# Kernel optimization log

Hardware: AMD Instinct MI355X
Metric: run time of the kernel (lower is better)

## Reference

```python
import jax, jax.numpy as jnp
import numpy as np
import math

B, S, E = 4, 2048, 1024
H, D = 16, 64

def setup_inputs() -> dict:
    key = jax.random.key(0)
    ks = jax.random.split(key, 9)
    sE = 1.0 / math.sqrt(E)
    sHD = 1.0 / math.sqrt(H * D)
    return {
        "x": jax.random.normal(ks[0], (B, S, E), jnp.float32),
        "Wq": jax.random.normal(ks[1], (H, E, D), jnp.float32) * sE,
        "bq": jax.random.normal(ks[2], (H, D), jnp.float32) * sE,
        "Wk": jax.random.normal(ks[3], (H, E, D), jnp.float32) * sE,
        "bk": jax.random.normal(ks[4], (H, D), jnp.float32) * sE,
        "Wv": jax.random.normal(ks[5], (H, E, D), jnp.float32) * sE,
        "bv": jax.random.normal(ks[6], (H, D), jnp.float32) * sE,
        "Wo": jax.random.normal(ks[7], (E, E), jnp.float32) * sHD,
        "bo": jax.random.normal(ks[8], (E,), jnp.float32) * sHD,
    }

def reference(x, Wq, bq, Wk, bk, Wv, bv, Wo, bo):
    # Projections for all heads at once: [B,H,S,D]
    Q = jnp.einsum('bse,hed->bhsd', x, Wq) + bq[:, None, :]
    K = jnp.einsum('bse,hed->bhsd', x, Wk) + bk[:, None, :]
    V = jnp.einsum('bse,hed->bhsd', x, Wv) + bv[:, None, :]
    scale = 1.0 / math.sqrt(D)
    scores = jnp.einsum('bhsd,bhtd->bhst', Q, K) * scale  # [B,H,S,S]
    S_len = x.shape[1]
    causal = jnp.tril(jnp.ones((S_len, S_len), dtype=bool))
    scores = jnp.where(causal, scores, -jnp.inf)
    probs = jax.nn.softmax(scores, axis=-1)
    ctx = jnp.einsum('bhst,bhtd->bhsd', probs, V)  # [B,H,S,D]
    # concat heads: head order matches torch cat over ModuleList
    conc = jnp.transpose(ctx, (0, 2, 1, 3)).reshape(x.shape[0], S_len, H * D)
    # torch Linear: y = conc @ W.T + b ; Wo stored as [out,in]=[E,E]
    out = conc @ Wo.T + bo
    # dropout is identity in eval mode
    return out
```

## Files before the change

kernel.cpp:

```cpp
#include <hip/hip_runtime.h>
#include <math.h>

constexpr int Bn = 4;
constexpr int Sn = 2048;
constexpr int En = 1024;
constexpr int Hn = 16;
constexpr int Dn = 64;

typedef float f32x4 __attribute__((ext_vector_type(4)));
typedef short s16x8 __attribute__((ext_vector_type(8)));
typedef short s16x4 __attribute__((ext_vector_type(4)));

__device__ __forceinline__ short f2bf(float f) {
    unsigned u = __builtin_bit_cast(unsigned, f);
    unsigned r = (u + 0x7fffu + ((u >> 16) & 1u)) >> 16;
    return (short)r;
}

__device__ __forceinline__ unsigned cvt_pk_bf16(float lo, float hi) {
    unsigned r;
    asm("v_cvt_pk_bf16_f32 %0, %1, %2" : "=v"(r) : "v"(lo), "v"(hi));
    return r;
}

__device__ __forceinline__ void glds16(const short* g, short* l) {
    __builtin_amdgcn_global_load_lds(
        (const __attribute__((address_space(1))) short*)g,
        (__attribute__((address_space(3))) short*)l, 16, 0, 0);
}

__global__ __launch_bounds__(256) void prep_kernel(
    const float* __restrict__ x, short* __restrict__ y,
    const float* __restrict__ Wq, const float* __restrict__ bq,
    const float* __restrict__ Wk, const float* __restrict__ bk,
    const float* __restrict__ Wv, const float* __restrict__ bv,
    short* __restrict__ Wcat, float* __restrict__ bias_cat,
    const float* __restrict__ Wo, short* __restrict__ Wob)
{
    const int bid = blockIdx.x;
    const int tid = threadIdx.x;

    if (bid < 8192) {
        size_t i = ((size_t)bid * 256 + tid) * 4;
        float4 v = *(const float4*)(x + i);
        s16x4 o;
        o[0] = f2bf(v.x); o[1] = f2bf(v.y); o[2] = f2bf(v.z); o[3] = f2bf(v.w);
        *(s16x4*)(y + i) = o;
    } else if (bid < 8960) {
        const int j  = bid - 8192;
        const int et = j & 15, h = (j >> 4) & 15, p = j >> 8;
        const float* W  = (p == 0) ? Wq : (p == 1) ? Wk : Wv;
        const float* bb = (p == 0) ? bq : (p == 1) ? bk : bv;
        const float* Wh = W + (size_t)h * En * Dn;

        __shared__ float T[64][65];
        #pragma unroll
        for (int it = 0; it < 16; it++) {
            int idx = tid + it * 256;
            int e = idx >> 6, d = idx & 63;
            T[d][e] = Wh[(size_t)(et * 64 + e) * Dn + d];
        }
        __syncthreads();
        #pragma unroll
        for (int it = 0; it < 16; it++) {
            int idx = tid + it * 256;
            int d = idx >> 6, e = idx & 63;
            Wcat[(size_t)(p * 1024 + h * 64 + d) * En + et * 64 + e] = f2bf(T[d][e]);
        }
        if (et == 0 && tid < 64)
            bias_cat[p * 1024 + h * 64 + tid] = bb[h * 64 + tid];
    } else {
        const size_t base = (size_t)(bid - 8960) * En;
        #pragma unroll
        for (int i = 0; i < 4; i++) {
            int k = tid + i * 256;
            Wob[base + k] = f2bf(Wo[base + k]);
        }
    }
}

__global__ __launch_bounds__(512) void gemm_bt_kernel(
    const short* __restrict__ A,
    const short* __restrict__ Bt,
    const float* __restrict__ bias,
    float* __restrict__ outF,
    short* __restrict__ Qb, short* __restrict__ Kb, short* __restrict__ Vtb,
    int mode)
{
    constexpr int K = En;
    const int m0 = blockIdx.x * 256;
    const int n0 = blockIdx.y * 128;

    __shared__ short As[256 * 64];
    __shared__ short Bs[128 * 64];

    const int tid  = threadIdx.x;
    const int w    = tid >> 6;
    const int lane = tid & 63;
    const int quad = lane >> 4;
    const int l15  = lane & 15;
    const int wr = (w >> 1) * 64;
    const int wc = (w & 1) * 64;

    f32x4 acc[4][4];
    #pragma unroll
    for (int i = 0; i < 4; i++)
        #pragma unroll
        for (int j = 0; j < 4; j++)
            #pragma unroll
            for (int e = 0; e < 4; e++) acc[i][j][e] = 0.f;

    for (int k0 = 0; k0 < K; k0 += 64) {
        #pragma unroll
        for (int r = 0; r < 4; r++) {
            int c   = (r * 8 + w) * 64 + lane;
            int row = c >> 3;
            int lp  = (c & 7) ^ (row & 7);
            glds16(A + (size_t)(m0 + row) * K + k0 + lp * 8,
                   As + (r * 8 + w) * 512);
        }
        #pragma unroll
        for (int r = 0; r < 2; r++) {
            int c   = (r * 8 + w) * 64 + lane;
            int row = c >> 3;
            int lp  = (c & 7) ^ (row & 7);
            glds16(Bt + (size_t)(n0 + row) * K + k0 + lp * 8,
                   Bs + (r * 8 + w) * 512);
        }
        __syncthreads();

        #pragma unroll
        for (int ks = 0; ks < 2; ks++) {
            s16x8 af[4], bfr[4];
            #pragma unroll
            for (int mt = 0; mt < 4; mt++) {
                int row = wr + mt * 16 + l15;
                af[mt] = *(const s16x8*)&As[row * 64 + (((ks * 4 + quad) ^ (l15 & 7)) * 8)];
            }
            #pragma unroll
            for (int nt = 0; nt < 4; nt++) {
                int row = wc + nt * 16 + l15;
                bfr[nt] = *(const s16x8*)&Bs[row * 64 + (((ks * 4 + quad) ^ (l15 & 7)) * 8)];
            }
            #pragma unroll
            for (int mt = 0; mt < 4; mt++)
                #pragma unroll
                for (int nt = 0; nt < 4; nt++)
                    acc[mt][nt] = __builtin_amdgcn_mfma_f32_16x16x32_bf16(
                        af[mt], bfr[nt], acc[mt][nt], 0, 0, 0);
        }
        __syncthreads();
    }

    if (mode == 0) {
        #pragma unroll
        for (int mt = 0; mt < 4; mt++) {
            #pragma unroll
            for (int reg = 0; reg < 4; reg++) {
                int m = m0 + wr + mt * 16 + quad * 4 + reg;
                #pragma unroll
                for (int nt = 0; nt < 4; nt++) {
                    int n = n0 + wc + nt * 16 + l15;
                    outF[(size_t)m * En + n] = acc[mt][nt][reg] + bias[n];
                }
            }
        }
    } else {
        const int p = (n0 + wc) >> 10;
        if (p < 2) {
            const float qs = (p == 0) ? 0.125f * 1.44269504088896f : 1.0f;
            short* dst = (p == 0) ? Qb : Kb;
            #pragma unroll
            for (int mt = 0; mt < 4; mt++) {
                #pragma unroll
                for (int reg = 0; reg < 4; reg++) {
                    int m = m0 + wr + mt * 16 + quad * 4 + reg;
                    int b = m >> 11, s = m & 2047;
                    #pragma unroll
                    for (int nt = 0; nt < 4; nt++) {
                        int n = n0 + wc + nt * 16 + l15;
                        int h = (n >> 6) & 15, d = n & 63;
                        dst[(((size_t)(b * Hn + h)) * Sn + s) * Dn + d] =
                            f2bf((acc[mt][nt][reg] + bias[n]) * qs);
                    }
                }
            }
        } else {
            #pragma unroll
            for (int mt = 0; mt < 4; mt++) {
                int m = m0 + wr + mt * 16 + quad * 4;
                int b = m >> 11, s = m & 2047;
                #pragma unroll
                for (int nt = 0; nt < 4; nt++) {
                    int n = n0 + wc + nt * 16 + l15;
                    int h = (n >> 6) & 15, d = n & 63;
                    s16x4 pk;
                    #pragma unroll
                    for (int reg = 0; reg < 4; reg++)
                        pk[reg] = f2bf(acc[mt][nt][reg] + bias[n]);
                    *(s16x4*)(Vtb + (((size_t)(b * Hn + h)) * Dn + d) * Sn + s) = pk;
                }
            }
        }
    }
}

__global__ __launch_bounds__(512) void gemm_bt_out_kernel(
    const short* __restrict__ A,
    const short* __restrict__ Bt,
    const float* __restrict__ bias,
    float* __restrict__ outF)
{
    constexpr int K = En;
    const int m0 = blockIdx.x * 128;
    const int n0 = blockIdx.y * 128;

    __shared__ short As[128 * 64];
    __shared__ short Bs[128 * 64];

    const int tid  = threadIdx.x;
    const int w    = tid >> 6;
    const int lane = tid & 63;
    const int quad = lane >> 4;
    const int l15  = lane & 15;
    const int wr = (w >> 1) * 32;
    const int wc = (w & 1) * 64;

    f32x4 acc[2][4];
    #pragma unroll
    for (int i = 0; i < 2; i++)
        #pragma unroll
        for (int j = 0; j < 4; j++)
            #pragma unroll
            for (int e = 0; e < 4; e++) acc[i][j][e] = 0.f;

    for (int k0 = 0; k0 < K; k0 += 64) {
        #pragma unroll
        for (int r = 0; r < 2; r++) {
            int c   = (r * 8 + w) * 64 + lane;
            int row = c >> 3;
            int lp  = (c & 7) ^ (row & 7);
            glds16(A + (size_t)(m0 + row) * K + k0 + lp * 8,
                   As + (r * 8 + w) * 512);
        }
        #pragma unroll
        for (int r = 0; r < 2; r++) {
            int c   = (r * 8 + w) * 64 + lane;
            int row = c >> 3;
            int lp  = (c & 7) ^ (row & 7);
            glds16(Bt + (size_t)(n0 + row) * K + k0 + lp * 8,
                   Bs + (r * 8 + w) * 512);
        }
        __syncthreads();

        #pragma unroll
        for (int ks = 0; ks < 2; ks++) {
            s16x8 af[2], bfr[4];
            #pragma unroll
            for (int mt = 0; mt < 2; mt++) {
                int row = wr + mt * 16 + l15;
                af[mt] = *(const s16x8*)&As[row * 64 + (((ks * 4 + quad) ^ (l15 & 7)) * 8)];
            }
            #pragma unroll
            for (int nt = 0; nt < 4; nt++) {
                int row = wc + nt * 16 + l15;
                bfr[nt] = *(const s16x8*)&Bs[row * 64 + (((ks * 4 + quad) ^ (l15 & 7)) * 8)];
            }
            #pragma unroll
            for (int mt = 0; mt < 2; mt++)
                #pragma unroll
                for (int nt = 0; nt < 4; nt++)
                    acc[mt][nt] = __builtin_amdgcn_mfma_f32_16x16x32_bf16(
                        af[mt], bfr[nt], acc[mt][nt], 0, 0, 0);
        }
        __syncthreads();
    }

    #pragma unroll
    for (int mt = 0; mt < 2; mt++) {
        #pragma unroll
        for (int reg = 0; reg < 4; reg++) {
            int m = m0 + wr + mt * 16 + quad * 4 + reg;
            #pragma unroll
            for (int nt = 0; nt < 4; nt++) {
                int n = n0 + wc + nt * 16 + l15;
                outF[(size_t)m * En + n] = acc[mt][nt][reg] + bias[n];
            }
        }
    }
}

__global__ __launch_bounds__(256, 8) void attn_mfma_kernel(
    const short* __restrict__ Q, const short* __restrict__ K,
    const short* __restrict__ Vt, short* __restrict__ Cb)
{
    constexpr int PP = 72;
    const int bid = blockIdx.x;
    const int kk  = bid >> 3;
    const int bh  = (bid & 7) * 8 + (kk >> 4);
    const int i   = kk & 15;
    const int b = bh >> 4, h = bh & 15;
    const int t0 = i, t1 = 31 - i;

    __shared__ short Ks[64 * 64];
    __shared__ short Vts[64 * 64];
    __shared__ short Ps[128 * PP];
    __shared__ float l_sh[128];

    const int tid  = threadIdx.x;
    const int w    = tid >> 6;
    const int lane = tid & 63;
    const int quad = lane >> 4;
    const int l15  = lane & 15;

    const short* Kp = K + (size_t)bh * Sn * Dn;
    const short* Vp = Vt + (size_t)bh * Dn * Sn;

    const int tf[2] = {t0, t1};
    s16x8 aq[2][2];
    #pragma unroll
    for (int f = 0; f < 2; f++)
        #pragma unroll
        for (int ks = 0; ks < 2; ks++)
            aq[f][ks] = *(const s16x8*)(
                Q + ((size_t)bh * Sn + tf[f] * 64 + w * 16 + l15) * Dn +
                ks * 32 + quad * 8);

    f32x4 acc[2][4];
    #pragma unroll
    for (int f = 0; f < 2; f++)
        #pragma unroll
        for (int nt = 0; nt < 4; nt++)
            #pragma unroll
            for (int e = 0; e < 4; e++) acc[f][nt][e] = 0.f;
    float lpart[2] = {0.f, 0.f};

    for (int kt = 0; kt <= t1; kt++) {
        #pragma unroll
        for (int r = 0; r < 2; r++) {
            int c   = (r * 4 + w) * 64 + lane;
            int row = c >> 3;
            int lp  = (c & 7) ^ (row & 7);
            glds16(Kp + (size_t)(kt * 64 + row) * Dn + lp * 8,
                   Ks + (r * 4 + w) * 512);
            glds16(Vp + (size_t)row * Sn + kt * 64 + lp * 8,
                   Vts + (r * 4 + w) * 512);
        }
        __syncthreads();

        #pragma unroll
        for (int f = 0; f < 2; f++) {
            if (kt > tf[f]) continue;
            f32x4 st[4];
            #pragma unroll
            for (int nt = 0; nt < 4; nt++)
                #pragma unroll
                for (int e = 0; e < 4; e++) st[nt][e] = 0.f;
            #pragma unroll
            for (int ks = 0; ks < 2; ks++) {
                #pragma unroll
                for (int nt = 0; nt < 4; nt++) {
                    s16x8 bk = *(const s16x8*)&Ks[(nt * 16 + l15) * 64 +
                                                  (((ks * 4 + quad) ^ (l15 & 7)) * 8)];
                    st[nt] = __builtin_amdgcn_mfma_f32_16x16x32_bf16(
                        bk, aq[f][ks], st[nt], 0, 0, 0);
                }
            }
            const bool diag = (kt == tf[f]);
            #pragma unroll
            for (int nt = 0; nt < 4; nt++) {
                float v[4];
                #pragma unroll
                for (int reg = 0; reg < 4; reg++) {
                    float e = __builtin_amdgcn_exp2f(st[nt][reg]);
                    if (diag && (nt * 16 + quad * 4 + reg) > (w * 16 + l15))
                        e = 0.f;
                    v[reg] = e;
                    lpart[f] += e;
                }
                uint2 pk;
                pk.x = cvt_pk_bf16(v[0], v[1]);
                pk.y = cvt_pk_bf16(v[2], v[3]);
                *(uint2*)&Ps[(f * 64 + w * 16 + l15) * PP + nt * 16 + quad * 4] = pk;
            }
        }

        #pragma unroll
        for (int ks = 0; ks < 2; ks++) {
            s16x8 bv[4];
            #pragma unroll
            for (int nt = 0; nt < 4; nt++)
                bv[nt] = *(const s16x8*)&Vts[(nt * 16 + l15) * 64 +
                                             (((ks * 4 + quad) ^ (l15 & 7)) * 8)];
            #pragma unroll
            for (int f = 0; f < 2; f++) {
                if (kt > tf[f]) continue;
                s16x8 ap = *(const s16x8*)&Ps[(f * 64 + w * 16 + l15) * PP +
                                              ks * 32 + quad * 8];
                #pragma unroll
                for (int nt = 0; nt < 4; nt++)
                    acc[f][nt] = __builtin_amdgcn_mfma_f32_16x16x32_bf16(
                        ap, bv[nt], acc[f][nt], 0, 0, 0);
            }
        }
        __syncthreads();
    }

    #pragma unroll
    for (int f = 0; f < 2; f++) {
        float l = lpart[f];
        l += __shfl_xor(l, 16);
        l += __shfl_xor(l, 32);
        if (quad == 0) l_sh[f * 64 + w * 16 + l15] = l;
    }
    __syncthreads();

    #pragma unroll
    for (int f = 0; f < 2; f++) {
        #pragma unroll
        for (int reg = 0; reg < 4; reg++) {
            int s = tf[f] * 64 + w * 16 + quad * 4 + reg;
            float inv = 1.f / l_sh[f * 64 + w * 16 + quad * 4 + reg];
            #pragma unroll
            for (int nt = 0; nt < 4; nt++) {
                int d = nt * 16 + l15;
                Cb[((size_t)(b * Sn + s)) * En + h * Dn + d] =
                    f2bf(acc[f][nt][reg] * inv);
            }
        }
    }
}

extern "C" void kernel_launch(void* const* d_in, const int* in_sizes, int n_in,
                              void* d_out, int out_size, void* d_ws, size_t ws_size,
                              hipStream_t stream) {
    const float* x  = (const float*)d_in[0];
    const float* Wq = (const float*)d_in[1];
    const float* bq = (const float*)d_in[2];
    const float* Wk = (const float*)d_in[3];
    const float* bk = (const float*)d_in[4];
    const float* Wv = (const float*)d_in[5];
    const float* bv = (const float*)d_in[6];
    const float* Wo = (const float*)d_in[7];
    const float* bo = (const float*)d_in[8];
    float* out = (float*)d_out;

    const size_t XS   = (size_t)Bn * Sn * En;
    const size_t WCS  = (size_t)3 * En * Hn * Dn;
    const size_t WOS  = (size_t)En * En;
    const size_t QSZ  = (size_t)Bn * Hn * Sn * Dn;

    short* Ax    = (short*)d_ws;
    short* Wcat  = Ax + XS;
    short* Wob   = Wcat + WCS;
    float* biasc = (float*)(Wob + WOS);
    short* Qb    = (short*)(biasc + 3072);
    short* Kb    = Qb + QSZ;
    short* Vtb   = Kb + QSZ;
    short* Cbf   = Vtb + QSZ;

    prep_kernel<<<dim3(8192 + 768 + 1024), 256, 0, stream>>>(
        x, Ax, Wq, bq, Wk, bk, Wv, bv, Wcat, biasc, Wo, Wob);

    gemm_bt_kernel<<<dim3((Bn * Sn) / 256, 3072 / 128), 512, 0, stream>>>(
        Ax, Wcat, biasc, nullptr, Qb, Kb, Vtb, 1);

    attn_mfma_kernel<<<dim3(16 * Bn * Hn), 256, 0, stream>>>(Qb, Kb, Vtb, Cbf);

    gemm_bt_out_kernel<<<dim3((Bn * Sn) / 128, En / 128), 512, 0, stream>>>(
        Cbf, Wob, bo, out);
}
```

Before: 244.9 us.

## Double-buffer K/V tiles in attention kernel with prefetch and vmcnt waits

The attention kernel now keeps two LDS buffers for K and V^T. It issues the global-to-LDS loads for tile kt+1 before computing on tile kt, waiting with s_waitcnt vmcnt(4) so that only the current tile's loads must finish. The aim is to hide global memory latency behind the MFMA and softmax work. The cost is double the K/V shared memory, which may lower occupancy under launch_bounds(256,8), and raw s_barrier with manual waitcnt is fragile if LDS write visibility is not guaranteed. The row sum is also reduced pairwise rather than serially.

After: 265.9 us. +8.6%, slower.

```diff
diff --git a/kernel.cpp b/kernel.cpp
--- a/kernel.cpp
+++ b/kernel.cpp
@@ -302,8 +302,8 @@
     const int b = bh >> 4, h = bh & 15;
     const int t0 = i, t1 = 31 - i;
 
-    __shared__ short Ks[64 * 64];
-    __shared__ short Vts[64 * 64];
+    __shared__ short Ks[2 * 64 * 64];
+    __shared__ short Vts[2 * 64 * 64];
     __shared__ short Ps[128 * PP];
     __shared__ float l_sh[128];
 
@@ -335,18 +335,37 @@
             for (int e = 0; e < 4; e++) acc[f][nt][e] = 0.f;
     float lpart[2] = {0.f, 0.f};
 
+    const int c0   = w * 64 + lane;
+    const int c1   = (4 + w) * 64 + lane;
+    const int row0 = c0 >> 3, lp0 = (c0 & 7) ^ (row0 & 7);
+    const int row1 = c1 >> 3, lp1 = (c1 & 7) ^ (row1 & 7);
+
+    #define STAGE(j, bufn)                                                    \
+        do {                                                                  \
+            glds16(Kp + (size_t)((j) * 64 + row0) * Dn + lp0 * 8,             \
+                   Ks + (bufn) * 4096 + w * 512);                             \
+            glds16(Vp + (size_t)row0 * Sn + (j) * 64 + lp0 * 8,               \
+                   Vts + (bufn) * 4096 + w * 512);                            \
+            glds16(Kp + (size_t)((j) * 64 + row1) * Dn + lp1 * 8,             \
+                   Ks + (bufn) * 4096 + (4 + w) * 512);                       \
+            glds16(Vp + (size_t)row1 * Sn + (j) * 64 + lp1 * 8,               \
+                   Vts + (bufn) * 4096 + (4 + w) * 512);                      \
+        } while (0)
+
+    STAGE(0, 0);
+
     for (int kt = 0; kt <= t1; kt++) {
-        #pragma unroll
-        for (int r = 0; r < 2; r++) {
-            int c   = (r * 4 + w) * 64 + lane;
-            int row = c >> 3;
-            int lp  = (c & 7) ^ (row & 7);
-            glds16(Kp + (size_t)(kt * 64 + row) * Dn + lp * 8,
-                   Ks + (r * 4 + w) * 512);
-            glds16(Vp + (size_t)row * Sn + kt * 64 + lp * 8,
-                   Vts + (r * 4 + w) * 512);
-        }
-        __syncthreads();
+        const int cur = kt & 1;
+        if (kt < t1) {
+            STAGE(kt + 1, cur ^ 1);
+            asm volatile("s_waitcnt vmcnt(4)" ::: "memory");
+        } else {
+            asm volatile("s_waitcnt vmcnt(0)" ::: "memory");
+        }
+        __builtin_amdgcn_s_barrier();
+
+        const short* Ksb  = Ks  + cur * 4096;
+        const short* Vtsb = Vts + cur * 4096;
 
         #pragma unroll
         for (int f = 0; f < 2; f++) {
@@ -360,8 +379,8 @@
             for (int ks = 0; ks < 2; ks++) {
                 #pragma unroll
                 for (int nt = 0; nt < 4; nt++) {
-                    s16x8 bk = *(const s16x8*)&Ks[(nt * 16 + l15) * 64 +
-                                                  (((ks * 4 + quad) ^ (l15 & 7)) * 8)];
+                    s16x8 bk = *(const s16x8*)&Ksb[(nt * 16 + l15) * 64 +
+                                                   (((ks * 4 + quad) ^ (l15 & 7)) * 8)];
                     st[nt] = __builtin_amdgcn_mfma_f32_16x16x32_bf16(
                         bk, aq[f][ks], st[nt], 0, 0, 0);
                 }
@@ -376,8 +395,8 @@
                     if (diag && (nt * 16 + quad * 4 + reg) > (w * 16 + l15))
                         e = 0.f;
                     v[reg] = e;
-                    lpart[f] += e;
                 }
+                lpart[f] += (v[0] + v[1]) + (v[2] + v[3]);
                 uint2 pk;
                 pk.x = cvt_pk_bf16(v[0], v[1]);
                 pk.y = cvt_pk_bf16(v[2], v[3]);
@@ -390,8 +409,8 @@
             s16x8 bv[4];
             #pragma unroll
             for (int nt = 0; nt < 4; nt++)
-                bv[nt] = *(const s16x8*)&Vts[(nt * 16 + l15) * 64 +
-                                             (((ks * 4 + quad) ^ (l15 & 7)) * 8)];
+                bv[nt] = *(const s16x8*)&Vtsb[(nt * 16 + l15) * 64 +
+                                              (((ks * 4 + quad) ^ (l15 & 7)) * 8)];
             #pragma unroll
             for (int f = 0; f < 2; f++) {
                 if (kt > tf[f]) continue;
@@ -403,8 +422,9 @@
                         ap, bv[nt], acc[f][nt], 0, 0, 0);
             }
         }
-        __syncthreads();
-    }
+        __builtin_amdgcn_s_barrier();
+    }
+    #undef STAGE
 
     #pragma unroll
     for (int f = 0; f < 2; f++) {
```

## Split paired causal query tiles into one tile per block, longest first

Applied to the files above, without the earlier changes.

The attention kernel previously gave each block a pair of query tiles (i and 31-i) so every block did balanced causal work while sharing each K/V tile load. Now each block handles a single 64-row query tile, and the grid doubles to 2048 blocks ordered so the longest tiles are dispatched first. This halves per-block LDS and register use, which can raise occupancy and improve scheduling. In exchange, K/V tiles are loaded once per query tile instead of once per pair, so global and L2 traffic increases.

Measured after the change: 241.9 us. Within noise of the previous version (-1.2%).

```diff
diff --git a/kernel.cpp b/kernel.cpp
--- a/kernel.cpp
+++ b/kernel.cpp
@@ -295,17 +295,17 @@
     const short* __restrict__ Vt, short* __restrict__ Cb)
 {
     constexpr int PP = 72;
-    const int bid = blockIdx.x;
-    const int kk  = bid >> 3;
-    const int bh  = (bid & 7) * 8 + (kk >> 4);
-    const int i   = kk & 15;
+    const int bid  = blockIdx.x;
+    const int slot = bid & 7;
+    const int j    = bid >> 3;
+    const int t    = 31 - (j >> 3);
+    const int bh   = slot * 8 + (j & 7);
     const int b = bh >> 4, h = bh & 15;
-    const int t0 = i, t1 = 31 - i;
 
     __shared__ short Ks[64 * 64];
     __shared__ short Vts[64 * 64];
-    __shared__ short Ps[128 * PP];
-    __shared__ float l_sh[128];
+    __shared__ short Ps[64 * PP];
+    __shared__ float l_sh[64];
 
     const int tid  = threadIdx.x;
     const int w    = tid >> 6;
@@ -316,26 +316,23 @@
     const short* Kp = K + (size_t)bh * Sn * Dn;
     const short* Vp = Vt + (size_t)bh * Dn * Sn;
 
-    const int tf[2] = {t0, t1};
-    s16x8 aq[2][2];
-    #pragma unroll
-    for (int f = 0; f < 2; f++)
-        #pragma unroll
-        for (int ks = 0; ks < 2; ks++)
-            aq[f][ks] = *(const s16x8*)(
-                Q + ((size_t)bh * Sn + tf[f] * 64 + w * 16 + l15) * Dn +
-                ks * 32 + quad * 8);
-
-    f32x4 acc[2][4];
-    #pragma unroll
-    for (int f = 0; f < 2; f++)
-        #pragma unroll
-        for (int nt = 0; nt < 4; nt++)
-            #pragma unroll
-            for (int e = 0; e < 4; e++) acc[f][nt][e] = 0.f;
-    float lpart[2] = {0.f, 0.f};
-
-    for (int kt = 0; kt <= t1; kt++) {
+    s16x8 aq[2];
+    #pragma unroll
+    for (int ks = 0; ks < 2; ks++)
+        aq[ks] = *(const s16x8*)(
+            Q + ((size_t)bh * Sn + t * 64 + w * 16 + l15) * Dn +
+            ks * 32 + quad * 8);
+
+    f32x4 acc[4];
+    #pragma unroll
+    for (int nt = 0; nt < 4; nt++)
+        #pragma unroll
+        for (int e = 0; e < 4; e++) acc[nt][e] = 0.f;
+    float lpart = 0.f;
+
+    const int prow = (w * 16 + l15) * PP;
+
+    for (int kt = 0; kt <= t; kt++) {
         #pragma unroll
         for (int r = 0; r < 2; r++) {
             int c   = (r * 4 + w) * 64 + lane;
@@ -348,85 +345,71 @@
         }
         __syncthreads();
 
-        #pragma unroll
-        for (int f = 0; f < 2; f++) {
-            if (kt > tf[f]) continue;
-            f32x4 st[4];
-            #pragma unroll
-            for (int nt = 0; nt < 4; nt++)
-                #pragma unroll
-                for (int e = 0; e < 4; e++) st[nt][e] = 0.f;
-            #pragma unroll
-            for (int ks = 0; ks < 2; ks++) {
-                #pragma unroll
-                for (int nt = 0; nt < 4; nt++) {
-                    s16x8 bk = *(const s16x8*)&Ks[(nt * 16 + l15) * 64 +
-                                                  (((ks * 4 + quad) ^ (l15 & 7)) * 8)];
-                    st[nt] = __builtin_amdgcn_mfma_f32_16x16x32_bf16(
-                        bk, aq[f][ks], st[nt], 0, 0, 0);
-                }
-            }
-            const bool diag = (kt == tf[f]);
+        f32x4 st[4];
+        #pragma unroll
+        for (int nt = 0; nt < 4; nt++)
+            #pragma unroll
+            for (int e = 0; e < 4; e++) st[nt][e] = 0.f;
+        #pragma unroll
+        for (int ks = 0; ks < 2; ks++) {
             #pragma unroll
             for (int nt = 0; nt < 4; nt++) {
-                float v[4];
-                #pragma unroll
-                for (int reg = 0; reg < 4; reg++) {
-                    float e = __builtin_amdgcn_exp2f(st[nt][reg]);
-                    if (diag && (nt * 16 + quad * 4 + reg) > (w * 16 + l15))
-                        e = 0.f;
-                    v[reg] = e;
-                    lpart[f] += e;
-                }
-                uint2 pk;
-                pk.x = cvt_pk_bf16(v[0], v[1]);
-                pk.y = cvt_pk_bf16(v[2], v[3]);
-                *(uint2*)&Ps[(f * 64 + w * 16 + l15) * PP + nt * 16 + quad * 4] = pk;
-            }
+                s16x8 bk = *(const s16x8*)&Ks[(nt * 16 + l15) * 64 +
+                                              (((ks * 4 + quad) ^ (l15 & 7)) * 8)];
+                st[nt] = __builtin_amdgcn_mfma_f32_16x16x32_bf16(
+                    bk, aq[ks], st[nt], 0, 0, 0);
+            }
+        }
+
+        const bool diag = (kt == t);
+        #pragma unroll
+        for (int nt = 0; nt < 4; nt++) {
+            float v[4];
+            #pragma unroll
+            for (int reg = 0; reg < 4; reg++) {
+                float e = __builtin_amdgcn_exp2f(st[nt][reg]);
+                if (diag && (nt * 16 + quad * 4 + reg) > (w * 16 + l15))
+                    e = 0.f;
+                v[reg] = e;
+                lpart += e;
+            }
+            uint2 pk;
+            pk.x = cvt_pk_bf16(v[0], v[1]);
+            pk.y = cvt_pk_bf16(v[2], v[3]);
+            *(uint2*)&Ps[prow + nt * 16 + quad * 4] = pk;
         }
 
         #pragma unroll
         for (int ks = 0; ks < 2; ks++) {
-            s16x8 bv[4];
-            #pragma unroll
-            for (int nt = 0; nt < 4; nt++)
-                bv[nt] = *(const s16x8*)&Vts[(nt * 16 + l15) * 64 +
-                                             (((ks * 4 + quad) ^ (l15 & 7)) * 8)];
-            #pragma unroll
-            for (int f = 0; f < 2; f++) {
-                if (kt > tf[f]) continue;
-                s16x8 ap = *(const s16x8*)&Ps[(f * 64 + w * 16 + l15) * PP +
-                                              ks * 32 + quad * 8];
-                #pragma unroll
-                for (int nt = 0; nt < 4; nt++)
-                    acc[f][nt] = __builtin_amdgcn_mfma_f32_16x16x32_bf16(
-                        ap, bv[nt], acc[f][nt], 0, 0, 0);
-            }
-        }
-        __syncthreads();
-    }
-
-    #pragma unroll
-    for (int f = 0; f < 2; f++) {
-        float l = lpart[f];
+            s16x8 ap = *(const s16x8*)&Ps[prow + ks * 32 + quad * 8];
+            #pragma unroll
+            for (int nt = 0; nt < 4; nt++) {
+                s16x8 bv = *(const s16x8*)&Vts[(nt * 16 + l15) * 64 +
+                                               (((ks * 4 + quad) ^ (l15 & 7)) * 8)];
+                acc[nt] = __builtin_amdgcn_mfma_f32_16x16x32_bf16(
+                    ap, bv, acc[nt], 0, 0, 0);
+            }
+        }
+        __syncthreads();
+    }
+
+    {
+        float l = lpart;
         l += __shfl_xor(l, 16);
         l += __shfl_xor(l, 32);
-        if (quad == 0) l_sh[f * 64 + w * 16 + l15] = l;
+        if (quad == 0) l_sh[w * 16 + l15] = l;
     }
     __syncthreads();
 
     #pragma unroll
-    for (int f = 0; f < 2; f++) {
-        #pragma unroll
-        for (int reg = 0; reg < 4; reg++) {
-            int s = tf[f] * 64 + w * 16 + quad * 4 + reg;
-            float inv = 1.f / l_sh[f * 64 + w * 16 + quad * 4 + reg];
-            #pragma unroll
-            for (int nt = 0; nt < 4; nt++) {
-                int d = nt * 16 + l15;
-                Cb[((size_t)(b * Sn + s)) * En + h * Dn + d] =
-                    f2bf(acc[f][nt][reg] * inv);
-            }
+    for (int reg = 0; reg < 4; reg++) {
+        int s = t * 64 + w * 16 + quad * 4 + reg;
+        float inv = 1.f / l_sh[w * 16 + quad * 4 + reg];
+        #pragma unroll
+        for (int nt = 0; nt < 4; nt++) {
+            int d = nt * 16 + l15;
+            Cb[((size_t)(b * Sn + s)) * En + h * Dn + d] =
+                f2bf(acc[nt][reg] * inv);
         }
     }
 }
@@ -465,7 +448,7 @@
     gemm_bt_kernel<<<dim3((Bn * Sn) / 256, 3072 / 128), 512, 0, stream>>>(
         Ax, Wcat, biasc, nullptr, Qb, Kb, Vtb, 1);
 
-    attn_mfma_kernel<<<dim3(16 * Bn * Hn), 256, 0, stream>>>(Qb, Kb, Vtb, Cbf);
+    attn_mfma_kernel<<<dim3(2048), 256, 0, stream>>>(Qb, Kb, Vtb, Cbf);
 
     gemm_bt_out_kernel<<<dim3((Bn * Sn) / 128, En / 128), 512, 0, stream>>>(
         Cbf, Wob, bo, out);
```
